# Performance work log

Measured on AMD Instinct MI355X. Metric: run time of the kernel, lower is better.

Reference implementation:

```python
import jax, jax.numpy as jnp
import numpy as np

B, N, E = 32, 1024, 16384
F_IN, H, C = 4, 4, 64
HC = H * C          # 256, concat head dim
FC0, FC1 = 128, 1
NEG_SLOPE = 0.2


def setup_inputs() -> dict:
    key = jax.random.key(0)
    ks = jax.random.split(key, 20)
    x = jax.random.normal(ks[0], (B, N, F_IN), dtype=jnp.float32)
    e = jax.random.normal(ks[1], (B, E, 1), dtype=jnp.float32)  # ignored by GATConv (edge_dim=None)
    edge_index0 = jax.random.randint(ks[2], (2, E), 0, N, dtype=jnp.int64)
    edge_index1 = jax.random.randint(ks[3], (2, E), 0, N, dtype=jnp.int64)

    def glorot(k, shape):
        fan = shape[0] + shape[-1]
        return jax.random.uniform(k, shape, jnp.float32, -1.0, 1.0) * np.sqrt(6.0 / fan)

    # GAT layer 0: F_IN -> (H, C)
    W0 = glorot(ks[4], (F_IN, HC))
    att_src0 = glorot(ks[5], (H, C))
    att_dst0 = glorot(ks[6], (H, C))
    b0 = jnp.zeros((HC,), jnp.float32)
    # GAT layer 1: HC -> (H, C)
    W1 = glorot(ks[7], (HC, HC))
    att_src1 = glorot(ks[8], (H, C))
    att_dst1 = glorot(ks[9], (H, C))
    b1 = jnp.zeros((HC,), jnp.float32)
    # FC head: 256 -> 128 -> ReLU -> 1 (no final ReLU: duplicate 'ReLU' module name)
    fc0_w = glorot(ks[10], (HC, FC0))
    fc0_b = jnp.zeros((FC0,), jnp.float32)
    fc1_w = glorot(ks[11], (FC0, FC1))
    fc1_b = jnp.zeros((FC1,), jnp.float32)
    return dict(x=x, e=e, edge_index0=edge_index0, edge_index1=edge_index1,
                W0=W0, att_src0=att_src0, att_dst0=att_dst0, b0=b0,
                W1=W1, att_src1=att_src1, att_dst1=att_dst1, b1=b1,
                fc0_w=fc0_w, fc0_b=fc0_b, fc1_w=fc1_w, fc1_b=fc1_b)


def _segment_softmax(logits, seg, num_segments):
    # softmax over edges grouped by target node, per head
    m = jax.ops.segment_max(logits, seg, num_segments=num_segments)
    m = jnp.where(jnp.isfinite(m), m, 0.0)
    ex = jnp.exp(logits - m[seg])
    s = jax.ops.segment_sum(ex, seg, num_segments=num_segments)
    return ex / (s[seg] + 1e-16)


def _gat_layer(xi, edge_index, W, att_src, att_dst, bias):
    # xi: (N, F_in); PyG GATConv, concat=True, add_self_loops=False
    h = (xi @ W).reshape(N, H, C)                 # (N, H, C)
    a_src = jnp.sum(h * att_src, axis=-1)         # (N, H)
    a_dst = jnp.sum(h * att_dst, axis=-1)         # (N, H)
    src, dst = edge_index[0], edge_index[1]       # message flows src -> dst
    alpha = jax.nn.leaky_relu(a_src[src] + a_dst[dst], NEG_SLOPE)  # (E, H)
    alpha = _segment_softmax(alpha, dst, N)
    msg = h[src] * alpha[:, :, None]              # (E, H, C)
    out = jax.ops.segment_sum(msg, dst, num_segments=N)  # (N, H, C)
    return out.reshape(N, HC) + bias


def reference(x, e, edge_index0, edge_index1,
              W0, att_src0, att_dst0, b0,
              W1, att_src1, att_dst1, b1,
              fc0_w, fc0_b, fc1_w, fc1_b):
    # edge_attr e is ignored (GATConv edge_dim=None), matching the original module
    def single(xi):
        y = _gat_layer(xi, edge_index0, W0, att_src0, att_dst0, b0)
        y = y + _gat_layer(y, edge_index1, W1, att_src1, att_dst1, b1)  # residual
        y = jax.nn.relu(y @ fc0_w + fc0_b)
        y = y @ fc1_w + fc1_b   # no final ReLU (duplicate module name in Sequential)
        return y                # (N, 1)
    return jax.vmap(single)(x)  # (B, N, 1)
```

## Files before the change

### kernel.cpp

```cpp
#include <hip/hip_runtime.h>

#define BB 32
#define NN 1024
#define EE 16384
#define HH 4
#define NEG 0.2f

__device__ __forceinline__ float4 f4(float v) { return make_float4(v, v, v, v); }
__device__ __forceinline__ float4 f4max(float4 a, float4 b) {
    return make_float4(fmaxf(a.x, b.x), fmaxf(a.y, b.y), fmaxf(a.z, b.z), fmaxf(a.w, b.w));
}
__device__ __forceinline__ float4 f4add(float4 a, float4 b) {
    return make_float4(a.x + b.x, a.y + b.y, a.z + b.z, a.w + b.w);
}
__device__ __forceinline__ float4 f4sub(float4 a, float4 b) {
    return make_float4(a.x - b.x, a.y - b.y, a.z - b.z, a.w - b.w);
}
__device__ __forceinline__ float4 f4mul(float4 a, float4 b) {
    return make_float4(a.x * b.x, a.y * b.y, a.z * b.z, a.w * b.w);
}
__device__ __forceinline__ float4 f4exp(float4 a) {
    return make_float4(__expf(a.x), __expf(a.y), __expf(a.z), __expf(a.w));
}
__device__ __forceinline__ float4 shflx4(float4 v, int o) {
    return make_float4(__shfl_xor(v.x, o), __shfl_xor(v.y, o),
                       __shfl_xor(v.z, o), __shfl_xor(v.w, o));
}
__device__ __forceinline__ float4 leaky4(float4 z) {
    return make_float4(z.x > 0.f ? z.x : NEG * z.x, z.y > 0.f ? z.y : NEG * z.y,
                       z.z > 0.f ? z.z : NEG * z.z, z.w > 0.f ? z.w : NEG * z.w);
}

__global__ __launch_bounds__(256) void k_count_prep1(
    const int* __restrict__ ei0, const int* __restrict__ ei1,
    int* __restrict__ cnt, const float* __restrict__ W0,
    const float* __restrict__ W1, const float* __restrict__ atts0,
    const float* __restrict__ attd0, const float* __restrict__ atts1,
    const float* __restrict__ attd1, float* __restrict__ ws1g,
    float* __restrict__ wd1g, float* __restrict__ ws0g,
    float* __restrict__ wd0g, float* __restrict__ Ug) {
    int blk = blockIdx.x, t = threadIdx.x;
    if (blk < 128) {
        int list = blk >> 6;
        int e = ((blk & 63) << 8) + t;
        const int* ei = list ? ei1 : ei0;
        atomicAdd(&cnt[(list << 10) + ei[EE + e]], 1);
        return;
    }
    int gid = ((blk - 128) << 8) + t;
    if (gid < 4096) {
        int i = gid >> 8, tt = gid & 255;
        int hp = i >> 2, f = i & 3;
        float a = 0.f;
        for (int c = 0; c < 64; ++c)
            a += W0[f * 256 + hp * 64 + c] * W1[(hp * 64 + c) * 256 + tt];
        Ug[i * 256 + tt] = a;
    } else if (gid < 5120) {
        int q = gid - 4096;
        int tt = q >> 2, h = q & 3;
        float a = 0.f;
        for (int c = 0; c < 64; ++c)
            a += W1[tt * 256 + h * 64 + c] * atts1[h * 64 + c];
        ws1g[q] = a;
    } else if (gid < 6144) {
        int q = gid - 5120;
        int tt = q >> 2, h = q & 3;
        float a = 0.f;
        for (int c = 0; c < 64; ++c)
            a += W1[tt * 256 + h * 64 + c] * attd1[h * 64 + c];
        wd1g[q] = a;
    } else if (gid < 6176) {
        int q = gid - 6144;
        int sel = q >> 4, i = q & 15;
        int f = i >> 2, h = i & 3;
        const float* att = sel ? attd0 : atts0;
        float a = 0.f;
        for (int c = 0; c < 64; ++c)
            a += W0[f * 256 + h * 64 + c] * att[h * 64 + c];
        (sel ? wd0g : ws0g)[i] = a;
    }
}

__global__ void k_scan2(int* __restrict__ cnt, int* __restrict__ off) {
    __shared__ int s[NN];
    int list = blockIdx.x;
    int* c = cnt + (list << 10);
    int* o = off + list * (NN + 1);
    int t = threadIdx.x;
    int v0 = c[t];
    s[t] = v0;
    __syncthreads();
    for (int d = 1; d < NN; d <<= 1) {
        int v = (t >= d) ? s[t - d] : 0;
        __syncthreads();
        s[t] += v;
        __syncthreads();
    }
    int excl = s[t] - v0;
    o[t] = excl;
    c[t] = excl;
    if (t == NN - 1) o[NN] = s[NN - 1];
}

__global__ __launch_bounds__(256) void k_scat_prep2_att0(
    const int* __restrict__ ei0, const int* __restrict__ ei1,
    int* __restrict__ cur, int* __restrict__ csr,
    const float* __restrict__ W0, const float* __restrict__ W1,
    const float* __restrict__ b0, const float* __restrict__ ws1g,
    const float* __restrict__ wd1g, float* __restrict__ Msg,
    float* __restrict__ Mdg, float* __restrict__ csg, float* __restrict__ cdg,
    float* __restrict__ bbw1, const float* __restrict__ x,
    const float* __restrict__ ws0g, const float* __restrict__ wd0g,
    float* __restrict__ as0, float* __restrict__ ad0) {
    int blk = blockIdx.x, t = threadIdx.x;
    if (blk < 128) {
        int list = blk >> 6;
        int e = ((blk & 63) << 8) + t;
        const int* ei = list ? ei1 : ei0;
        int sv = ei[e];
        int d = ei[EE + e];
        int p = atomicAdd(&cur[(list << 10) + d], 1);
        csr[(list << 14) + p] = sv;
        return;
    }
    if (blk < 130) {
        int gid = ((blk - 128) << 8) + t;
        if (gid < 64) {
            int i = gid >> 2, h = gid & 3;
            int hp = i >> 2, f = i & 3;
            float a = 0.f;
            for (int c = 0; c < 64; ++c)
                a += W0[f * 256 + hp * 64 + c] * ws1g[(hp * 64 + c) * 4 + h];
            Msg[gid] = a;
        } else if (gid < 128) {
            int q = gid - 64;
            int i = q >> 2, h = q & 3;
            int hp = i >> 2, f = i & 3;
            float a = 0.f;
            for (int c = 0; c < 64; ++c)
                a += W0[f * 256 + hp * 64 + c] * wd1g[(hp * 64 + c) * 4 + h];
            Mdg[q] = a;
        } else if (gid < 132) {
            int h = gid - 128;
            float a = 0.f;
            for (int tt = 0; tt < 256; ++tt) a += b0[tt] * ws1g[tt * 4 + h];
            csg[h] = a;
        } else if (gid < 136) {
            int h = gid - 132;
            float a = 0.f;
            for (int tt = 0; tt < 256; ++tt) a += b0[tt] * wd1g[tt * 4 + h];
            cdg[h] = a;
        } else if (gid >= 256) {
            int tt = gid - 256;
            float a = 0.f;
            for (int tp = 0; tp < 256; ++tp) a += b0[tp] * W1[tp * 256 + tt];
            bbw1[tt] = a;
        }
        return;
    }
    int bn = ((blk - 130) << 8) + t;
    float4 xv = *(const float4*)&x[bn << 2];
    float4 s, d;
    s.x = xv.x * ws0g[0] + xv.y * ws0g[4] + xv.z * ws0g[8] + xv.w * ws0g[12];
    s.y = xv.x * ws0g[1] + xv.y * ws0g[5] + xv.z * ws0g[9] + xv.w * ws0g[13];
    s.z = xv.x * ws0g[2] + xv.y * ws0g[6] + xv.z * ws0g[10] + xv.w * ws0g[14];
    s.w = xv.x * ws0g[3] + xv.y * ws0g[7] + xv.z * ws0g[11] + xv.w * ws0g[15];
    d.x = xv.x * wd0g[0] + xv.y * wd0g[4] + xv.z * wd0g[8] + xv.w * wd0g[12];
    d.y = xv.x * wd0g[1] + xv.y * wd0g[5] + xv.z * wd0g[9] + xv.w * wd0g[13];
    d.z = xv.x * wd0g[2] + xv.y * wd0g[6] + xv.z * wd0g[10] + xv.w * wd0g[14];
    d.w = xv.x * wd0g[3] + xv.y * wd0g[7] + xv.z * wd0g[11] + xv.w * wd0g[15];
    *(float4*)&as0[bn << 2] = s;
    *(float4*)&ad0[bn << 2] = d;
}

__global__ __launch_bounds__(256) void k_agg0_prepB(
    const float* __restrict__ x, const float* __restrict__ as0,
    const float* __restrict__ ad0, const int* __restrict__ off,
    const int* __restrict__ csr, const float* __restrict__ Msg,
    const float* __restrict__ Mdg, const float* __restrict__ csg,
    const float* __restrict__ cdg, float* __restrict__ xbar,
    float* __restrict__ as1, float* __restrict__ ad1,
    const float* __restrict__ W0, const float* __restrict__ fc0w,
    const float* __restrict__ fc0b, const float* __restrict__ b0,
    const float* __restrict__ b1, const float* __restrict__ bbw1,
    const float* __restrict__ Ug, float* __restrict__ Wcat,
    float* __restrict__ c2a, float* __restrict__ c2b) {
    int blk = blockIdx.x, t = threadIdx.x;
    if (blk >= 2048) {
        int gid = ((blk - 2048) << 8) + t;
        if (gid < 8192) {
            int row = gid >> 7, u = gid & 127;
            int h = row >> 4, j = row & 15;
            float a = 0.f;
            for (int c = 0; c < 64; ++c)
                a += Ug[j * 256 + h * 64 + c] * fc0w[(h * 64 + c) * 128 + u];
            Wcat[row * 128 + u] = a;
        } else if (gid < 10240) {
            int row = gid >> 7, u = gid & 127;
            int j = row - 64;
            int h = j >> 2, f = j & 3;
            float a = 0.f;
            for (int c = 0; c < 64; ++c)
                a += W0[f * 256 + h * 64 + c] * fc0w[(h * 64 + c) * 128 + u];
            Wcat[row * 128 + u] = a;
        } else if (gid < 10368) {
            int u = gid - 10240;
            float a = fc0b[u];
            for (int tt = 0; tt < 256; ++tt)
                a += (b1[tt] + b0[tt]) * fc0w[tt * 128 + u];
            c2a[u] = a;
        } else if (gid < 10496) {
            int u = gid - 10368;
            float a = 0.f;
            for (int tt = 0; tt < 256; ++tt) a += bbw1[tt] * fc0w[tt * 128 + u];
            c2b[u] = a;
        }
        return;
    }
    int g = t >> 4, l = t & 15;
    int bn = (blk << 4) + g;
    int b = bn >> 10, n = bn & (NN - 1);
    int beg = off[n], end = off[n + 1];
    float4 adv = *(const float4*)&ad0[bn << 2];
    float4 m4 = f4(-1e30f), den = f4(0.f);
    float pacc[16];
#pragma unroll
    for (int i = 0; i < 16; ++i) pacc[i] = 0.f;
    for (int base = beg + l; base < end; base += 16) {
        int s = csr[base];
        float4 av = *(const float4*)&as0[((b << 10) + s) << 2];
        float4 xs = *(const float4*)&x[((b << 10) + s) << 2];
        float4 lv = leaky4(f4add(av, adv));
        float4 nm = f4max(m4, lv);
        float4 r = f4exp(f4sub(m4, nm));
        float4 ex = f4exp(f4sub(lv, nm));
        m4 = nm;
        den = f4add(f4mul(den, r), ex);
        float rr[4] = {r.x, r.y, r.z, r.w};
        float exa[4] = {ex.x, ex.y, ex.z, ex.w};
        float xsa[4] = {xs.x, xs.y, xs.z, xs.w};
#pragma unroll
        for (int i = 0; i < 16; ++i)
            pacc[i] = pacc[i] * rr[i >> 2] + exa[i >> 2] * xsa[i & 3];
    }
    float4 ml = m4;
#pragma unroll
    for (int o = 8; o; o >>= 1) m4 = f4max(m4, shflx4(m4, o));
    float4 sc = f4exp(f4sub(ml, m4));
    den = f4mul(den, sc);
    float sca[4] = {sc.x, sc.y, sc.z, sc.w};
#pragma unroll
    for (int i = 0; i < 16; ++i) pacc[i] *= sca[i >> 2];
#pragma unroll
    for (int o = 8; o; o >>= 1) {
        den = f4add(den, shflx4(den, o));
#pragma unroll
        for (int i = 0; i < 16; ++i) pacc[i] += __shfl_xor(pacc[i], o);
    }
    float iva[4] = {1.f / (den.x + 1e-16f), 1.f / (den.y + 1e-16f),
                    1.f / (den.z + 1e-16f), 1.f / (den.w + 1e-16f)};
    float xbn[16];
#pragma unroll
    for (int i = 0; i < 16; ++i) xbn[i] = pacc[i] * iva[i >> 2];
    if (l == 0) {
#pragma unroll
        for (int q = 0; q < 4; ++q) {
            float4 v = make_float4(xbn[q * 4], xbn[q * 4 + 1], xbn[q * 4 + 2],
                                   xbn[q * 4 + 3]);
            *(float4*)&xbar[(bn << 4) + (q << 2)] = v;
        }
    }
    if (l < 8) {
        int h = l & 3, sel = l >> 2;
        const float* M = sel ? Mdg : Msg;
        float a = sel ? cdg[h] : csg[h];
#pragma unroll
        for (int i = 0; i < 16; ++i) a += xbn[i] * M[i * 4 + h];
        (sel ? ad1 : as1)[(bn << 2) + h] = a;
    }
}

__global__ __launch_bounds__(256) void k_agg1(
    const float* __restrict__ xbar, const float* __restrict__ as1,
    const float* __restrict__ ad1, const int* __restrict__ off,
    const int* __restrict__ csr, float* __restrict__ xb2) {
    int t = threadIdx.x;
    int wid = t >> 6, tw = t & 63;
    int h = tw >> 4, slot = tw & 15;
    int bn = (blockIdx.x << 2) + wid;
    int b = bn >> 10, n = bn & (NN - 1);
    int beg = off[n], end = off[n + 1];
    float adh = ad1[(bn << 2) + h];
    float ml = -1e30f, den = 0.f;
    float pacc[16];
#pragma unroll
    for (int i = 0; i < 16; ++i) pacc[i] = 0.f;
    const float* xbb = xbar + ((size_t)b << 14);
    for (int base = beg + slot; base < end; base += 16) {
        int s = csr[base];
        float av = as1[(((b << 10) + s) << 2) + h];
        float z = av + adh;
        float lv = z > 0.f ? z : NEG * z;
        float nm = fmaxf(ml, lv);
        float r = __expf(ml - nm);
        float ex = __expf(lv - nm);
        ml = nm;
        den = den * r + ex;
        const float* xp = xbb + (s << 4);
        float4 x0 = *(const float4*)(xp);
        float4 x1 = *(const float4*)(xp + 4);
        float4 x2 = *(const float4*)(xp + 8);
        float4 x3 = *(const float4*)(xp + 12);
        float xsa[16] = {x0.x, x0.y, x0.z, x0.w, x1.x, x1.y, x1.z, x1.w,
                         x2.x, x2.y, x2.z, x2.w, x3.x, x3.y, x3.z, x3.w};
#pragma unroll
        for (int i = 0; i < 16; ++i) pacc[i] = pacc[i] * r + ex * xsa[i];
    }
    float M = ml;
#pragma unroll
    for (int o = 8; o; o >>= 1) M = fmaxf(M, __shfl_xor(M, o));
    float sc = __expf(ml - M);
    den *= sc;
#pragma unroll
    for (int i = 0; i < 16; ++i) pacc[i] *= sc;
#pragma unroll
    for (int o = 8; o; o >>= 1) {
        den += __shfl_xor(den, o);
#pragma unroll
        for (int i = 0; i < 16; ++i) pacc[i] += __shfl_xor(pacc[i], o);
    }
    float inv = 1.f / (den + 1e-16f);
    if (slot == 0) {
#pragma unroll
        for (int q = 0; q < 4; ++q) {
            float4 v = make_float4(pacc[q * 4] * inv, pacc[q * 4 + 1] * inv,
                                   pacc[q * 4 + 2] * inv, pacc[q * 4 + 3] * inv);
            *(float4*)&xb2[(bn << 6) + (h << 4) + (q << 2)] = v;
        }
    }
}

#define AP 132
__global__ __launch_bounds__(256) void k_final(
    const float* __restrict__ xbar, const float* __restrict__ xb2,
    const float* __restrict__ Wcat, const float* __restrict__ c2a,
    const float* __restrict__ c2b, const float* __restrict__ fc1w,
    const float* __restrict__ fc1b, const int* __restrict__ off1,
    float* __restrict__ out) {
    __shared__ float Bs[80 * 128];
    __shared__ float As[80 * AP];
    __shared__ float c2as[128], c2bs[128], f1s[128];
    int t = threadIdx.x;
    int nb0 = blockIdx.x << 7;
    for (int i = t; i < 2560; i += 256) {
        float4 v = *(const float4*)&Wcat[i << 2];
        *(float4*)&Bs[i << 2] = v;
    }
    if (t < 128) {
        c2as[t] = c2a[t];
        c2bs[t] = c2b[t];
        f1s[t] = fc1w[t];
    }
#pragma unroll
    for (int i = 0; i < 8; ++i) {
        int q = t + (i << 8);
        int node = q >> 4, kq = q & 15;
        float4 v = *(const float4*)&xb2[((nb0 + node) << 6) + (kq << 2)];
        As[(kq * 4 + 0) * AP + node] = v.x;
        As[(kq * 4 + 1) * AP + node] = v.y;
        As[(kq * 4 + 2) * AP + node] = v.z;
        As[(kq * 4 + 3) * AP + node] = v.w;
    }
#pragma unroll
    for (int i = 0; i < 2; ++i) {
        int q = t + (i << 8);
        int node = q >> 2, kq = q & 3;
        float4 v = *(const float4*)&xbar[((nb0 + node) << 4) + (kq << 2)];
        As[(64 + kq * 4 + 0) * AP + node] = v.x;
        As[(64 + kq * 4 + 1) * AP + node] = v.y;
        As[(64 + kq * 4 + 2) * AP + node] = v.z;
        As[(64 + kq * 4 + 3) * AP + node] = v.w;
    }
    __syncthreads();
    int tx = t & 15, ty = t >> 4;
    int u0 = tx << 3, n0 = ty << 3;
    float za[8][8];
#pragma unroll
    for (int i = 0; i < 8; ++i)
#pragma unroll
        for (int j = 0; j < 8; ++j) za[i][j] = 0.f;
#pragma unroll 4
    for (int k = 0; k < 80; ++k) {
        float4 alo = *(const float4*)&As[k * AP + n0];
        float4 ahi = *(const float4*)&As[k * AP + n0 + 4];
        float4 blo = *(const float4*)&Bs[(k << 7) + u0];
        float4 bhi = *(const float4*)&Bs[(k << 7) + u0 + 4];
        float aa[8] = {alo.x, alo.y, alo.z, alo.w, ahi.x, ahi.y, ahi.z, ahi.w};
        float bb[8] = {blo.x, blo.y, blo.z, blo.w, bhi.x, bhi.y, bhi.z, bhi.w};
#pragma unroll
        for (int i = 0; i < 8; ++i)
#pragma unroll
            for (int j = 0; j < 8; ++j) za[i][j] += aa[i] * bb[j];
    }
    float fb = fc1b[0];
#pragma unroll
    for (int i = 0; i < 8; ++i) {
        int bnn = nb0 + n0 + i;
        int nl = bnn & (NN - 1);
        int deg = off1[nl + 1] - off1[nl];
        float part = 0.f;
#pragma unroll
        for (int j = 0; j < 8; ++j) {
            int u = u0 + j;
            float z = za[i][j] + c2as[u] + (deg > 0 ? c2bs[u] : 0.f);
            z = z > 0.f ? z : 0.f;
            part += z * f1s[u];
        }
#pragma unroll
        for (int o = 8; o; o >>= 1) part += __shfl_xor(part, o);
        if (tx == 0) out[bnn] = part + fb;
    }
}

extern "C" void kernel_launch(void* const* d_in, const int* in_sizes, int n_in,
                              void* d_out, int out_size, void* d_ws, size_t ws_size,
                              hipStream_t stream) {
    const float* x = (const float*)d_in[0];
    const int* ei0 = (const int*)d_in[2];
    const int* ei1 = (const int*)d_in[3];
    const float* W0 = (const float*)d_in[4];
    const float* atts0 = (const float*)d_in[5];
    const float* attd0 = (const float*)d_in[6];
    const float* b0 = (const float*)d_in[7];
    const float* W1 = (const float*)d_in[8];
    const float* atts1 = (const float*)d_in[9];
    const float* attd1 = (const float*)d_in[10];
    const float* b1 = (const float*)d_in[11];
    const float* fc0w = (const float*)d_in[12];
    const float* fc0b = (const float*)d_in[13];
    const float* fc1w = (const float*)d_in[14];
    const float* fc1b = (const float*)d_in[15];
    float* out = (float*)d_out;

    float* fw = (float*)d_ws;
    float* xbar = fw;                 fw += (size_t)BB * NN * 16;
    float* xb2 = fw;                  fw += (size_t)BB * NN * 64;
    float* as0 = fw;                  fw += (size_t)BB * NN * 4;
    float* ad0 = fw;                  fw += (size_t)BB * NN * 4;
    float* as1 = fw;                  fw += (size_t)BB * NN * 4;
    float* ad1 = fw;                  fw += (size_t)BB * NN * 4;
    float* Ug = fw;                   fw += 4096;
    float* Wcat = fw;                 fw += 80 * 128;
    float* bbw1 = fw;                 fw += 256;
    float* c2a = fw;                  fw += 128;
    float* c2b = fw;                  fw += 128;
    float* ws0g = fw;                 fw += 16;
    float* wd0g = fw;                 fw += 16;
    float* Msg = fw;                  fw += 64;
    float* Mdg = fw;                  fw += 64;
    float* csg = fw;                  fw += 4;
    float* cdg = fw;                  fw += 4;
    float* ws1g = fw;                 fw += 1024;
    float* wd1g = fw;                 fw += 1024;
    int* ip = (int*)fw;
    int* off = ip;                    ip += 2 * (NN + 1);
    int* cnt = ip;                    ip += 2 * NN;
    int* csr = ip;

    hipMemsetAsync(cnt, 0, 2 * NN * sizeof(int), stream);
    k_count_prep1<<<153, 256, 0, stream>>>(ei0, ei1, cnt, W0, W1, atts0, attd0,
                                           atts1, attd1, ws1g, wd1g, ws0g,
                                           wd0g, Ug);
    k_scan2<<<2, NN, 0, stream>>>(cnt, off);
    k_scat_prep2_att0<<<258, 256, 0, stream>>>(
        ei0, ei1, cnt, csr, W0, W1, b0, ws1g, wd1g, Msg, Mdg, csg, cdg, bbw1,
        x, ws0g, wd0g, as0, ad0);
    k_agg0_prepB<<<2089, 256, 0, stream>>>(
        x, as0, ad0, off, csr, Msg, Mdg, csg, cdg, xbar, as1, ad1, W0, fc0w,
        fc0b, b0, b1, bbw1, Ug, Wcat, c2a, c2b);
    k_agg1<<<BB * NN / 4, 256, 0, stream>>>(xbar, as1, ad1, off + (NN + 1),
                                            csr + EE, xb2);
    k_final<<<BB * NN / 128, 256, 0, stream>>>(xbar, xb2, Wcat, c2a, c2b, fc1w,
                                               fc1b, off + (NN + 1), out);
}
```

Before: 178.3 us.

## Fuse layer-1 aggregation with FC head and recompute layer-0 attention on the fly

Merges the layer-1 aggregation kernel with the final FC head, so aggregated features stay in shared memory and the xb2 global buffer is no longer written and read back. Layer-0 attention scores are recomputed from x inside the aggregation kernel instead of being stored in as0/ad0. The prep work is reshuffled across kernels: scan is combined with prep2 and the Wcat prep moves into the scatter kernel. Each 512-thread block of the fused kernel now reloads the whole 40KB Wcat matrix into shared memory, and the FC matmul becomes per-node dot products rather than a register-tiled GEMM.

```diff
diff --git a/kernel.cpp b/kernel.cpp
--- a/kernel.cpp
+++ b/kernel.cpp
@@ -3,7 +3,6 @@
 #define BB 32
 #define NN 1024
 #define EE 16384
-#define HH 4
 #define NEG 0.2f
 
 __device__ __forceinline__ float4 f4(float v) { return make_float4(v, v, v, v); }
@@ -81,37 +80,77 @@
     }
 }
 
-__global__ void k_scan2(int* __restrict__ cnt, int* __restrict__ off) {
-    __shared__ int s[NN];
-    int list = blockIdx.x;
-    int* c = cnt + (list << 10);
-    int* o = off + list * (NN + 1);
-    int t = threadIdx.x;
-    int v0 = c[t];
-    s[t] = v0;
-    __syncthreads();
-    for (int d = 1; d < NN; d <<= 1) {
-        int v = (t >= d) ? s[t - d] : 0;
-        __syncthreads();
-        s[t] += v;
-        __syncthreads();
-    }
-    int excl = s[t] - v0;
-    o[t] = excl;
-    c[t] = excl;
-    if (t == NN - 1) o[NN] = s[NN - 1];
-}
-
-__global__ __launch_bounds__(256) void k_scat_prep2_att0(
-    const int* __restrict__ ei0, const int* __restrict__ ei1,
-    int* __restrict__ cur, int* __restrict__ csr,
+__global__ __launch_bounds__(1024) void k_scan_prep2(
+    int* __restrict__ cnt, int* __restrict__ off,
     const float* __restrict__ W0, const float* __restrict__ W1,
     const float* __restrict__ b0, const float* __restrict__ ws1g,
     const float* __restrict__ wd1g, float* __restrict__ Msg,
     float* __restrict__ Mdg, float* __restrict__ csg, float* __restrict__ cdg,
-    float* __restrict__ bbw1, const float* __restrict__ x,
-    const float* __restrict__ ws0g, const float* __restrict__ wd0g,
-    float* __restrict__ as0, float* __restrict__ ad0) {
+    float* __restrict__ bbw1) {
+    int blk = blockIdx.x, t = threadIdx.x;
+    if (blk < 2) {
+        __shared__ int s[NN];
+        int* c = cnt + (blk << 10);
+        int* o = off + blk * (NN + 1);
+        int v0 = c[t];
+        s[t] = v0;
+        __syncthreads();
+        for (int d = 1; d < NN; d <<= 1) {
+            int v = (t >= d) ? s[t - d] : 0;
+            __syncthreads();
+            s[t] += v;
+            __syncthreads();
+        }
+        int excl = s[t] - v0;
+        o[t] = excl;
+        c[t] = excl;
+        if (t == NN - 1) o[NN] = s[NN - 1];
+        return;
+    }
+    if (blk == 2) {
+        if (t < 64) {
+            int i = t >> 2, h = t & 3;
+            int hp = i >> 2, f = i & 3;
+            float a = 0.f;
+            for (int c = 0; c < 64; ++c)
+                a += W0[f * 256 + hp * 64 + c] * ws1g[(hp * 64 + c) * 4 + h];
+            Msg[t] = a;
+        } else if (t < 128) {
+            int q = t - 64;
+            int i = q >> 2, h = q & 3;
+            int hp = i >> 2, f = i & 3;
+            float a = 0.f;
+            for (int c = 0; c < 64; ++c)
+                a += W0[f * 256 + hp * 64 + c] * wd1g[(hp * 64 + c) * 4 + h];
+            Mdg[q] = a;
+        } else if (t < 132) {
+            int h = t - 128;
+            float a = 0.f;
+            for (int tt = 0; tt < 256; ++tt) a += b0[tt] * ws1g[tt * 4 + h];
+            csg[h] = a;
+        } else if (t < 136) {
+            int h = t - 132;
+            float a = 0.f;
+            for (int tt = 0; tt < 256; ++tt) a += b0[tt] * wd1g[tt * 4 + h];
+            cdg[h] = a;
+        }
+        return;
+    }
+    if (t < 256) {
+        float a = 0.f;
+        for (int tp = 0; tp < 256; ++tp) a += b0[tp] * W1[tp * 256 + t];
+        bbw1[t] = a;
+    }
+}
+
+__global__ __launch_bounds__(256) void k_scat_prepB(
+    const int* __restrict__ ei0, const int* __restrict__ ei1,
+    int* __restrict__ cur, int* __restrict__ csr,
+    const float* __restrict__ W0, const float* __restrict__ fc0w,
+    const float* __restrict__ fc0b, const float* __restrict__ b0,
+    const float* __restrict__ b1, const float* __restrict__ bbw1,
+    const float* __restrict__ Ug, float* __restrict__ Wcat,
+    float* __restrict__ c2a, float* __restrict__ c2b) {
     int blk = blockIdx.x, t = threadIdx.x;
     if (blk < 128) {
         int list = blk >> 6;
@@ -123,113 +162,72 @@
         csr[(list << 14) + p] = sv;
         return;
     }
-    if (blk < 130) {
-        int gid = ((blk - 128) << 8) + t;
-        if (gid < 64) {
-            int i = gid >> 2, h = gid & 3;
-            int hp = i >> 2, f = i & 3;
-            float a = 0.f;
-            for (int c = 0; c < 64; ++c)
-                a += W0[f * 256 + hp * 64 + c] * ws1g[(hp * 64 + c) * 4 + h];
-            Msg[gid] = a;
-        } else if (gid < 128) {
-            int q = gid - 64;
-            int i = q >> 2, h = q & 3;
-            int hp = i >> 2, f = i & 3;
-            float a = 0.f;
-            for (int c = 0; c < 64; ++c)
-                a += W0[f * 256 + hp * 64 + c] * wd1g[(hp * 64 + c) * 4 + h];
-            Mdg[q] = a;
-        } else if (gid < 132) {
-            int h = gid - 128;
-            float a = 0.f;
-            for (int tt = 0; tt < 256; ++tt) a += b0[tt] * ws1g[tt * 4 + h];
-            csg[h] = a;
-        } else if (gid < 136) {
-            int h = gid - 132;
-            float a = 0.f;
-            for (int tt = 0; tt < 256; ++tt) a += b0[tt] * wd1g[tt * 4 + h];
-            cdg[h] = a;
-        } else if (gid >= 256) {
-            int tt = gid - 256;
-            float a = 0.f;
-            for (int tp = 0; tp < 256; ++tp) a += b0[tp] * W1[tp * 256 + tt];
-            bbw1[tt] = a;
-        }
-        return;
-    }
-    int bn = ((blk - 130) << 8) + t;
-    float4 xv = *(const float4*)&x[bn << 2];
-    float4 s, d;
-    s.x = xv.x * ws0g[0] + xv.y * ws0g[4] + xv.z * ws0g[8] + xv.w * ws0g[12];
-    s.y = xv.x * ws0g[1] + xv.y * ws0g[5] + xv.z * ws0g[9] + xv.w * ws0g[13];
-    s.z = xv.x * ws0g[2] + xv.y * ws0g[6] + xv.z * ws0g[10] + xv.w * ws0g[14];
-    s.w = xv.x * ws0g[3] + xv.y * ws0g[7] + xv.z * ws0g[11] + xv.w * ws0g[15];
-    d.x = xv.x * wd0g[0] + xv.y * wd0g[4] + xv.z * wd0g[8] + xv.w * wd0g[12];
-    d.y = xv.x * wd0g[1] + xv.y * wd0g[5] + xv.z * wd0g[9] + xv.w * wd0g[13];
-    d.z = xv.x * wd0g[2] + xv.y * wd0g[6] + xv.z * wd0g[10] + xv.w * wd0g[14];
-    d.w = xv.x * wd0g[3] + xv.y * wd0g[7] + xv.z * wd0g[11] + xv.w * wd0g[15];
-    *(float4*)&as0[bn << 2] = s;
-    *(float4*)&ad0[bn << 2] = d;
-}
-
-__global__ __launch_bounds__(256) void k_agg0_prepB(
-    const float* __restrict__ x, const float* __restrict__ as0,
-    const float* __restrict__ ad0, const int* __restrict__ off,
-    const int* __restrict__ csr, const float* __restrict__ Msg,
+    int gid = ((blk - 128) << 8) + t;
+    if (gid < 8192) {
+        int row = gid >> 7, u = gid & 127;
+        int h = row >> 4, j = row & 15;
+        float a = 0.f;
+        for (int c = 0; c < 64; ++c)
+            a += Ug[j * 256 + h * 64 + c] * fc0w[(h * 64 + c) * 128 + u];
+        Wcat[row * 128 + u] = a;
+    } else if (gid < 10240) {
+        int row = gid >> 7, u = gid & 127;
+        int j = row - 64;
+        int h = j >> 2, f = j & 3;
+        float a = 0.f;
+        for (int c = 0; c < 64; ++c)
+            a += W0[f * 256 + h * 64 + c] * fc0w[(h * 64 + c) * 128 + u];
+        Wcat[row * 128 + u] = a;
+    } else if (gid < 10368) {
+        int u = gid - 10240;
+        float a = fc0b[u];
+        for (int tt = 0; tt < 256; ++tt)
+            a += (b1[tt] + b0[tt]) * fc0w[tt * 128 + u];
+        c2a[u] = a;
+    } else if (gid < 10496) {
+        int u = gid - 10368;
+        float a = 0.f;
+        for (int tt = 0; tt < 256; ++tt) a += bbw1[tt] * fc0w[tt * 128 + u];
+        c2b[u] = a;
+    }
+}
+
+__global__ __launch_bounds__(256) void k_agg0(
+    const float* __restrict__ x, const int* __restrict__ off,
+    const int* __restrict__ csr, const float* __restrict__ ws0g,
+    const float* __restrict__ wd0g, const float* __restrict__ Msg,
     const float* __restrict__ Mdg, const float* __restrict__ csg,
     const float* __restrict__ cdg, float* __restrict__ xbar,
-    float* __restrict__ as1, float* __restrict__ ad1,
-    const float* __restrict__ W0, const float* __restrict__ fc0w,
-    const float* __restrict__ fc0b, const float* __restrict__ b0,
-    const float* __restrict__ b1, const float* __restrict__ bbw1,
-    const float* __restrict__ Ug, float* __restrict__ Wcat,
-    float* __restrict__ c2a, float* __restrict__ c2b) {
-    int blk = blockIdx.x, t = threadIdx.x;
-    if (blk >= 2048) {
-        int gid = ((blk - 2048) << 8) + t;
-        if (gid < 8192) {
-            int row = gid >> 7, u = gid & 127;
-            int h = row >> 4, j = row & 15;
-            float a = 0.f;
-            for (int c = 0; c < 64; ++c)
-                a += Ug[j * 256 + h * 64 + c] * fc0w[(h * 64 + c) * 128 + u];
-            Wcat[row * 128 + u] = a;
-        } else if (gid < 10240) {
-            int row = gid >> 7, u = gid & 127;
-            int j = row - 64;
-            int h = j >> 2, f = j & 3;
-            float a = 0.f;
-            for (int c = 0; c < 64; ++c)
-                a += W0[f * 256 + h * 64 + c] * fc0w[(h * 64 + c) * 128 + u];
-            Wcat[row * 128 + u] = a;
-        } else if (gid < 10368) {
-            int u = gid - 10240;
-            float a = fc0b[u];
-            for (int tt = 0; tt < 256; ++tt)
-                a += (b1[tt] + b0[tt]) * fc0w[tt * 128 + u];
-            c2a[u] = a;
-        } else if (gid < 10496) {
-            int u = gid - 10368;
-            float a = 0.f;
-            for (int tt = 0; tt < 256; ++tt) a += bbw1[tt] * fc0w[tt * 128 + u];
-            c2b[u] = a;
-        }
-        return;
-    }
+    float* __restrict__ as1, float* __restrict__ ad1) {
+    int t = threadIdx.x;
     int g = t >> 4, l = t & 15;
-    int bn = (blk << 4) + g;
+    int bn = (blockIdx.x << 4) + g;
     int b = bn >> 10, n = bn & (NN - 1);
     int beg = off[n], end = off[n + 1];
-    float4 adv = *(const float4*)&ad0[bn << 2];
+    float ws[16], wd[16];
+#pragma unroll
+    for (int i = 0; i < 16; ++i) {
+        ws[i] = ws0g[i];
+        wd[i] = wd0g[i];
+    }
+    float4 xd = *(const float4*)&x[bn << 2];
+    float4 adv;
+    adv.x = xd.x * wd[0] + xd.y * wd[4] + xd.z * wd[8] + xd.w * wd[12];
+    adv.y = xd.x * wd[1] + xd.y * wd[5] + xd.z * wd[9] + xd.w * wd[13];
+    adv.z = xd.x * wd[2] + xd.y * wd[6] + xd.z * wd[10] + xd.w * wd[14];
+    adv.w = xd.x * wd[3] + xd.y * wd[7] + xd.z * wd[11] + xd.w * wd[15];
     float4 m4 = f4(-1e30f), den = f4(0.f);
     float pacc[16];
 #pragma unroll
     for (int i = 0; i < 16; ++i) pacc[i] = 0.f;
     for (int base = beg + l; base < end; base += 16) {
         int s = csr[base];
-        float4 av = *(const float4*)&as0[((b << 10) + s) << 2];
         float4 xs = *(const float4*)&x[((b << 10) + s) << 2];
+        float4 av;
+        av.x = xs.x * ws[0] + xs.y * ws[4] + xs.z * ws[8] + xs.w * ws[12];
+        av.y = xs.x * ws[1] + xs.y * ws[5] + xs.z * ws[9] + xs.w * ws[13];
+        av.z = xs.x * ws[2] + xs.y * ws[6] + xs.z * ws[10] + xs.w * ws[14];
+        av.w = xs.x * ws[3] + xs.y * ws[7] + xs.z * ws[11] + xs.w * ws[15];
         float4 lv = leaky4(f4add(av, adv));
         float4 nm = f4max(m4, lv);
         float4 r = f4exp(f4sub(m4, nm));
@@ -280,16 +278,31 @@
     }
 }
 
-__global__ __launch_bounds__(256) void k_agg1(
+__global__ __launch_bounds__(512) void k_agg1_final(
     const float* __restrict__ xbar, const float* __restrict__ as1,
     const float* __restrict__ ad1, const int* __restrict__ off,
-    const int* __restrict__ csr, float* __restrict__ xb2) {
+    const int* __restrict__ csr, const float* __restrict__ Wcat,
+    const float* __restrict__ c2a, const float* __restrict__ c2b,
+    const float* __restrict__ fc1w, const float* __restrict__ fc1b,
+    float* __restrict__ out) {
+    __shared__ float Ws[80 * 128];
+    __shared__ float As[8][88];
+    __shared__ float c2as[128], c2bs[128], f1s[128];
+    __shared__ int degs[8];
     int t = threadIdx.x;
+    for (int i = t; i < 2560; i += 512)
+        *(float4*)&Ws[i << 2] = *(const float4*)&Wcat[i << 2];
+    if (t < 128) {
+        c2as[t] = c2a[t];
+        c2bs[t] = c2b[t];
+        f1s[t] = fc1w[t];
+    }
     int wid = t >> 6, tw = t & 63;
     int h = tw >> 4, slot = tw & 15;
-    int bn = (blockIdx.x << 2) + wid;
+    int bn = (blockIdx.x << 3) + wid;
     int b = bn >> 10, n = bn & (NN - 1);
     int beg = off[n], end = off[n + 1];
+    if (tw == 0) degs[wid] = end - beg;
     float adh = ad1[(bn << 2) + h];
     float ml = -1e30f, den = 0.f;
     float pacc[16];
@@ -335,91 +348,29 @@
         for (int q = 0; q < 4; ++q) {
             float4 v = make_float4(pacc[q * 4] * inv, pacc[q * 4 + 1] * inv,
                                    pacc[q * 4 + 2] * inv, pacc[q * 4 + 3] * inv);
-            *(float4*)&xb2[(bn << 6) + (h << 4) + (q << 2)] = v;
+            *(float4*)&As[wid][(h << 4) + (q << 2)] = v;
         }
     }
-}
-
-#define AP 132
-__global__ __launch_bounds__(256) void k_final(
-    const float* __restrict__ xbar, const float* __restrict__ xb2,
-    const float* __restrict__ Wcat, const float* __restrict__ c2a,
-    const float* __restrict__ c2b, const float* __restrict__ fc1w,
-    const float* __restrict__ fc1b, const int* __restrict__ off1,
-    float* __restrict__ out) {
-    __shared__ float Bs[80 * 128];
-    __shared__ float As[80 * AP];
-    __shared__ float c2as[128], c2bs[128], f1s[128];
-    int t = threadIdx.x;
-    int nb0 = blockIdx.x << 7;
-    for (int i = t; i < 2560; i += 256) {
-        float4 v = *(const float4*)&Wcat[i << 2];
-        *(float4*)&Bs[i << 2] = v;
-    }
-    if (t < 128) {
-        c2as[t] = c2a[t];
-        c2bs[t] = c2b[t];
-        f1s[t] = fc1w[t];
-    }
-#pragma unroll
-    for (int i = 0; i < 8; ++i) {
-        int q = t + (i << 8);
-        int node = q >> 4, kq = q & 15;
-        float4 v = *(const float4*)&xb2[((nb0 + node) << 6) + (kq << 2)];
-        As[(kq * 4 + 0) * AP + node] = v.x;
-        As[(kq * 4 + 1) * AP + node] = v.y;
-        As[(kq * 4 + 2) * AP + node] = v.z;
-        As[(kq * 4 + 3) * AP + node] = v.w;
-    }
-#pragma unroll
-    for (int i = 0; i < 2; ++i) {
-        int q = t + (i << 8);
-        int node = q >> 2, kq = q & 3;
-        float4 v = *(const float4*)&xbar[((nb0 + node) << 4) + (kq << 2)];
-        As[(64 + kq * 4 + 0) * AP + node] = v.x;
-        As[(64 + kq * 4 + 1) * AP + node] = v.y;
-        As[(64 + kq * 4 + 2) * AP + node] = v.z;
-        As[(64 + kq * 4 + 3) * AP + node] = v.w;
+    if (tw < 4) {
+        float4 v = *(const float4*)&xbar[(bn << 4) + (tw << 2)];
+        *(float4*)&As[wid][64 + (tw << 2)] = v;
     }
     __syncthreads();
-    int tx = t & 15, ty = t >> 4;
-    int u0 = tx << 3, n0 = ty << 3;
-    float za[8][8];
-#pragma unroll
-    for (int i = 0; i < 8; ++i)
-#pragma unroll
-        for (int j = 0; j < 8; ++j) za[i][j] = 0.f;
-#pragma unroll 4
+    int hasdeg = degs[wid] > 0;
+    float z0 = c2as[tw] + (hasdeg ? c2bs[tw] : 0.f);
+    float z1 = c2as[tw + 64] + (hasdeg ? c2bs[tw + 64] : 0.f);
+#pragma unroll 8
     for (int k = 0; k < 80; ++k) {
-        float4 alo = *(const float4*)&As[k * AP + n0];
-        float4 ahi = *(const float4*)&As[k * AP + n0 + 4];
-        float4 blo = *(const float4*)&Bs[(k << 7) + u0];
-        float4 bhi = *(const float4*)&Bs[(k << 7) + u0 + 4];
-        float aa[8] = {alo.x, alo.y, alo.z, alo.w, ahi.x, ahi.y, ahi.z, ahi.w};
-        float bb[8] = {blo.x, blo.y, blo.z, blo.w, bhi.x, bhi.y, bhi.z, bhi.w};
-#pragma unroll
-        for (int i = 0; i < 8; ++i)
-#pragma unroll
-            for (int j = 0; j < 8; ++j) za[i][j] += aa[i] * bb[j];
-    }
-    float fb = fc1b[0];
-#pragma unroll
-    for (int i = 0; i < 8; ++i) {
-        int bnn = nb0 + n0 + i;
-        int nl = bnn & (NN - 1);
-        int deg = off1[nl + 1] - off1[nl];
-        float part = 0.f;
-#pragma unroll
-        for (int j = 0; j < 8; ++j) {
-            int u = u0 + j;
-            float z = za[i][j] + c2as[u] + (deg > 0 ? c2bs[u] : 0.f);
-            z = z > 0.f ? z : 0.f;
-            part += z * f1s[u];
-        }
-#pragma unroll
-        for (int o = 8; o; o >>= 1) part += __shfl_xor(part, o);
-        if (tx == 0) out[bnn] = part + fb;
-    }
+        float a = As[wid][k];
+        z0 += a * Ws[(k << 7) + tw];
+        z1 += a * Ws[(k << 7) + tw + 64];
+    }
+    z0 = z0 > 0.f ? z0 : 0.f;
+    z1 = z1 > 0.f ? z1 : 0.f;
+    float part = z0 * f1s[tw] + z1 * f1s[tw + 64];
+#pragma unroll
+    for (int o = 32; o; o >>= 1) part += __shfl_xor(part, o);
+    if (tw == 0) out[bn] = part + fc1b[0];
 }
 
 extern "C" void kernel_launch(void* const* d_in, const int* in_sizes, int n_in,
@@ -444,9 +395,6 @@
 
     float* fw = (float*)d_ws;
     float* xbar = fw;                 fw += (size_t)BB * NN * 16;
-    float* xb2 = fw;                  fw += (size_t)BB * NN * 64;
-    float* as0 = fw;                  fw += (size_t)BB * NN * 4;
-    float* ad0 = fw;                  fw += (size_t)BB * NN * 4;
     float* as1 = fw;                  fw += (size_t)BB * NN * 4;
     float* ad1 = fw;                  fw += (size_t)BB * NN * 4;
     float* Ug = fw;                   fw += 4096;
@@ -471,15 +419,13 @@
     k_count_prep1<<<153, 256, 0, stream>>>(ei0, ei1, cnt, W0, W1, atts0, attd0,
                                            atts1, attd1, ws1g, wd1g, ws0g,
                                            wd0g, Ug);
-    k_scan2<<<2, NN, 0, stream>>>(cnt, off);
-    k_scat_prep2_att0<<<258, 256, 0, stream>>>(
-        ei0, ei1, cnt, csr, W0, W1, b0, ws1g, wd1g, Msg, Mdg, csg, cdg, bbw1,
-        x, ws0g, wd0g, as0, ad0);
-    k_agg0_prepB<<<2089, 256, 0, stream>>>(
-        x, as0, ad0, off, csr, Msg, Mdg, csg, cdg, xbar, as1, ad1, W0, fc0w,
-        fc0b, b0, b1, bbw1, Ug, Wcat, c2a, c2b);
-    k_agg1<<<BB * NN / 4, 256, 0, stream>>>(xbar, as1, ad1, off + (NN + 1),
-                                            csr + EE, xb2);
-    k_final<<<BB * NN / 128, 256, 0, stream>>>(xbar, xb2, Wcat, c2a, c2b, fc1w,
-                                               fc1b, off + (NN + 1), out);
-}
+    k_scan_prep2<<<4, 1024, 0, stream>>>(cnt, off, W0, W1, b0, ws1g, wd1g,
+                                         Msg, Mdg, csg, cdg, bbw1);
+    k_scat_prepB<<<169, 256, 0, stream>>>(ei0, ei1, cnt, csr, W0, fc0w, fc0b,
+                                          b0, b1, bbw1, Ug, Wcat, c2a, c2b);
+    k_agg0<<<BB * NN / 16, 256, 0, stream>>>(x, off, csr, ws0g, wd0g, Msg, Mdg,
+                                             csg, cdg, xbar, as1, ad1);
+    k_agg1_final<<<BB * NN / 8, 512, 0, stream>>>(
+        xbar, as1, ad1, off + (NN + 1), csr + EE, Wcat, c2a, c2b, fc1w, fc1b,
+        out);
+}
```

Result: slower. 197.7 us (+10.9%).
